# Kernel optimization log

Measured on AMD Instinct MI355X. Metric: run time of the kernel, lower is better.

The kernel has to match this reference:

```python
import jax, jax.numpy as jnp
import numpy as np

B, T, C, H = 65536, 100, 7, 2  # batch, timesteps, covariates, lstm hidden


def setup_inputs() -> dict:
    key = jax.random.key(0)
    ks = iter(jax.random.split(key, 32))
    def rn(shape, s=0.1):
        return jax.random.normal(next(ks), shape, dtype=jnp.float32) * s
    inp = {"x": jax.random.normal(next(ks), (B, T, C), dtype=jnp.float32)}
    for l, din in ((0, C), (1, 2 * H)):
        for suf in ("", "r"):
            inp[f"w_ih_l{l}{suf}"] = rn((4 * H, din))
            inp[f"w_hh_l{l}{suf}"] = rn((4 * H, H))
            inp[f"b_ih_l{l}{suf}"] = rn((4 * H,))
            inp[f"b_hh_l{l}{suf}"] = rn((4 * H,))
    inp["fc1_w"] = rn((64, 4 * T))
    inp["fc1_b"] = rn((64,))
    inp["fc2_w"] = rn((20, 64))
    inp["fc2_b"] = rn((20,))
    return inp


def _lstm_dir(xw, w_hh, b_hh, reverse):
    # xw: [T, B, 4H] precomputed input projection (x @ W_ih.T + b_ih)
    if reverse:
        xw = xw[::-1]
    h0 = jnp.zeros((xw.shape[1], H), xw.dtype)
    c0 = jnp.zeros((xw.shape[1], H), xw.dtype)

    def step(carry, gx):
        h, c = carry
        g = gx + h @ w_hh.T + b_hh            # [B, 4H]
        i, f, gg, o = jnp.split(g, 4, axis=-1)  # torch gate order i,f,g,o
        c = jax.nn.sigmoid(f) * c + jax.nn.sigmoid(i) * jnp.tanh(gg)
        h = jax.nn.sigmoid(o) * jnp.tanh(c)
        return (h, c), h

    _, hs = jax.lax.scan(step, (h0, c0), xw)
    if reverse:
        hs = hs[::-1]
    return hs  # [T, B, H]


def _bilstm_layer(x_tbf, w_ih_f, w_hh_f, b_ih_f, b_hh_f,
                  w_ih_b, w_hh_b, b_ih_b, b_hh_b):
    xw_f = jnp.einsum('tbc,gc->tbg', x_tbf, w_ih_f) + b_ih_f
    xw_b = jnp.einsum('tbc,gc->tbg', x_tbf, w_ih_b) + b_ih_b
    hf = _lstm_dir(xw_f, w_hh_f, b_hh_f, False)
    hb = _lstm_dir(xw_b, w_hh_b, b_hh_b, True)
    return jnp.concatenate([hf, hb], axis=-1)  # [T, B, 2H]


def reference(x,
              w_ih_l0, w_hh_l0, b_ih_l0, b_hh_l0,
              w_ih_l0r, w_hh_l0r, b_ih_l0r, b_hh_l0r,
              w_ih_l1, w_hh_l1, b_ih_l1, b_hh_l1,
              w_ih_l1r, w_hh_l1r, b_ih_l1r, b_hh_l1r,
              fc1_w, fc1_b, fc2_w, fc2_b):
    xt = jnp.transpose(x.reshape(-1, T, C), (1, 0, 2))  # [T, B, C] time-major
    h1 = _bilstm_layer(xt, w_ih_l0, w_hh_l0, b_ih_l0, b_hh_l0,
                       w_ih_l0r, w_hh_l0r, b_ih_l0r, b_hh_l0r)
    h2 = _bilstm_layer(h1, w_ih_l1, w_hh_l1, b_ih_l1, b_hh_l1,
                       w_ih_l1r, w_hh_l1r, b_ih_l1r, b_hh_l1r)
    out = jnp.transpose(h2, (1, 0, 2)).reshape(-1, 4 * T)  # flatten [B, 4T]
    out = jax.nn.relu(out)                  # relu BEFORE fc1, as in original
    out = jax.nn.relu(out @ fc1_w.T + fc1_b)
    return out @ fc2_w.T + fc2_b            # [B, 20]
```

## Files before the change

### kernel.cpp

```cpp
#include <hip/hip_runtime.h>

#define Bn 65536
#define Tn 100
#define Cn 7

typedef short short8 __attribute__((ext_vector_type(8)));
typedef float float4v __attribute__((ext_vector_type(4)));

__device__ __forceinline__ float fast_rcp(float x) { return __builtin_amdgcn_rcpf(x); }
__device__ __forceinline__ float sig_f(float x) { return fast_rcp(1.f + __expf(-x)); }
__device__ __forceinline__ float tanh_f(float x) { return 1.f - 2.f * fast_rcp(__expf(2.f * x) + 1.f); }
__device__ __forceinline__ unsigned bf16rne(float x) {
    unsigned u = __float_as_uint(x);
    return (u + 0x7fffu + ((u >> 16) & 1u)) >> 16;
}

typedef const __attribute__((address_space(1))) void* gp_t;
typedef __attribute__((address_space(3))) void* sp_t;
__device__ __forceinline__ void async_copy_dw(const float* g, float* l) {
    __builtin_amdgcn_global_load_lds((gp_t)g, (sp_t)l, 4, 0, 0);
}

__global__ void w2prep_kernel(const float* __restrict__ fc1_w, unsigned short* __restrict__ w2g) {
    int idx = blockIdx.x * 256 + threadIdx.x;
    int w = idx >> 13, d = (idx >> 12) & 1, n = (idx >> 6) & 63, kk = idx & 63;
    int tt = kk >> 1, i = kk & 1;
    int t = d ? (99 - 25 * w - tt) : (25 * w + tt);
    float v = (kk < 50) ? fc1_w[n * 400 + 4 * t + 2 * d + i] : 0.f;
    w2g[idx] = (unsigned short)bf16rne(v);
}

__global__ __launch_bounds__(256) void l0_kernel(
    const float* __restrict__ x,
    const float* __restrict__ wih_f, const float* __restrict__ whh_f,
    const float* __restrict__ bih_f, const float* __restrict__ bhh_f,
    const float* __restrict__ wih_r, const float* __restrict__ whh_r,
    const float* __restrict__ bih_r, const float* __restrict__ bhh_r,
    float2* __restrict__ h1f2)
{
    __shared__ float xs[2][2][4480];

    const int tid  = threadIdx.x;
    const int rev  = tid >> 7;
    const int s    = tid & 127;
    const int b    = blockIdx.x * 128 + s;
    const int w    = tid >> 6;
    const int lane = tid & 63;
    const int sdir = w >> 1;
    const int half = w & 1;

    const float* wih = rev ? wih_r : wih_f;
    const float* whh = rev ? whh_r : whh_f;
    const float* bih = rev ? bih_r : bih_f;
    const float* bhh = rev ? bhh_r : bhh_f;

    float wi[56], wh[16], bias[8];
#pragma unroll
    for (int k = 0; k < 56; ++k) wi[k] = wih[k];
#pragma unroll
    for (int k = 0; k < 16; ++k) wh[k] = whh[k];
#pragma unroll
    for (int k = 0; k < 8; ++k) bias[k] = bih[k] + bhh[k];

    const int e  = (lane >= 35) ? 1 : 0;
    const int r0 = lane - 35 * e;
    const int s0 = half * 64 + e;
    const float* xsamp = x + (size_t)(blockIdx.x * 128 + s0) * 700;

    auto stage = [&](int ch, int p) {
        const int off = sdir ? (665 - 35 * ch) : (35 * ch);
        const float* g = xsamp + off + r0;
        float* l = &xs[p][sdir][half * 2240 + lane];
        int r = r0;
#pragma unroll
        for (int i = 0; i < 35; ++i) {
            async_copy_dw(g, l);
            l += 64;
            const int c = (r >= 6) ? 1 : 0;
            g += c ? 1394 : 729;
            r += c ? -6 : 29;
        }
    };

    float h0 = 0.f, h1v = 0.f, c0 = 0.f, c1 = 0.f;

    stage(0, 0);
#pragma unroll 1
    for (int ch = 0; ch < 20; ++ch) {
        __builtin_amdgcn_s_waitcnt(0);
        __syncthreads();
        if (ch < 19) stage(ch + 1, (ch + 1) & 1);

        const int t0 = rev ? (95 - 5 * ch) : (5 * ch);
        const float* xbuf = &xs[ch & 1][rev][0];
#pragma unroll 1
        for (int tt = 0; tt < 5; ++tt) {
            const int rr = rev ? (4 - tt) : tt;
            const int t  = t0 + rr;
            const float* xrow = xbuf + s * 35 + rr * 7;

            float g[8];
#pragma unroll
            for (int k = 0; k < 8; ++k) g[k] = bias[k];
#pragma unroll
            for (int c = 0; c < 7; ++c) {
                const float xv = xrow[c];
#pragma unroll
                for (int k = 0; k < 8; ++k) g[k] = fmaf(wi[k * 7 + c], xv, g[k]);
            }
#pragma unroll
            for (int k = 0; k < 8; ++k)
                g[k] = fmaf(wh[k * 2], h0, fmaf(wh[k * 2 + 1], h1v, g[k]));

            const float i0 = sig_f(g[0]), i1 = sig_f(g[1]);
            const float f0 = sig_f(g[2]), f1 = sig_f(g[3]);
            const float q0 = tanh_f(g[4]), q1 = tanh_f(g[5]);
            const float o0 = sig_f(g[6]), o1 = sig_f(g[7]);
            c0 = fmaf(f0, c0, i0 * q0);
            c1 = fmaf(f1, c1, i1 * q1);
            h0  = o0 * tanh_f(c0);
            h1v = o1 * tanh_f(c1);

            h1f2[((size_t)t * 2 + rev) * Bn + b] = make_float2(h0, h1v);
        }
    }
}

__global__ __launch_bounds__(256) void l1fc_kernel(
    const float2* __restrict__ hin,
    const float* __restrict__ wih_f, const float* __restrict__ whh_f,
    const float* __restrict__ bih_f, const float* __restrict__ bhh_f,
    const float* __restrict__ wih_r, const float* __restrict__ whh_r,
    const float* __restrict__ bih_r, const float* __restrict__ bhh_r,
    const float4* __restrict__ w2g,
    const float* __restrict__ fc1_b,
    const float* __restrict__ fc2_w,
    const float* __restrict__ fc2_b,
    float* __restrict__ out)
{
    __shared__ unsigned a2[2 * 128 * 36];
    __shared__ unsigned w2[2 * 64 * 36];

    const int tid  = threadIdx.x;
    const int ww   = tid >> 6;
    const int lane = tid & 63;
    const int d    = ww >> 1;
    const int half = ww & 1;
    const int sm   = half * 64 + lane;
    const size_t b = (size_t)blockIdx.x * 128 + sm;

    const float* wih = d ? wih_r : wih_f;
    const float* whh = d ? whh_r : whh_f;
    const float* bih = d ? bih_r : bih_f;
    const float* bhh = d ? bhh_r : bhh_f;

    float wi[32], wh[16], bias[8];
#pragma unroll
    for (int k = 0; k < 32; ++k) wi[k] = wih[k];
#pragma unroll
    for (int k = 0; k < 16; ++k) wh[k] = whh[k];
#pragma unroll
    for (int k = 0; k < 8; ++k) bias[k] = bih[k] + bhh[k];

    float4v acc[2][4];
#pragma unroll
    for (int mt = 0; mt < 2; ++mt)
#pragma unroll
        for (int nt = 0; nt < 4; ++nt) acc[mt][nt] = (float4v){0.f, 0.f, 0.f, 0.f};

    for (int i2 = tid; i2 < 2 * 128 * 36; i2 += 256) a2[i2] = 0u;
    __syncthreads();

    auto tstep = [&](int st) { return d ? 99 - st : st; };
    auto hload = [&](int t, float2& uF, float2& uR) {
        uF = hin[((size_t)t * 2) * Bn + b];
        uR = hin[((size_t)t * 2 + 1) * Bn + b];
    };

    float2 aF, aR, p1F, p1R, p2F, p2R;
    hload(tstep(0), aF, aR);
    hload(tstep(1), p1F, p1R);
    hload(tstep(2), p2F, p2R);

    float h0 = 0.f, h1v = 0.f, c0 = 0.f, c1 = 0.f;
    const int cbase = tid * 4;

#pragma unroll 1
    for (int w = 0; w < 4; ++w) {
        float4 wl[4];
#pragma unroll
        for (int j = 0; j < 4; ++j) wl[j] = w2g[w * 1024 + cbase + j];

#pragma unroll 1
        for (int tt = 0; tt < 25; ++tt) {
            const int st = 25 * w + tt;
            const int sp = (st + 3 <= 99) ? st + 3 : 99;
            float2 nF, nR;
            hload(tstep(sp), nF, nR);

            float g[8];
#pragma unroll
            for (int k = 0; k < 8; ++k) {
                g[k] = bias[k];
                g[k] = fmaf(wi[k * 4 + 0], aF.x, g[k]);
                g[k] = fmaf(wi[k * 4 + 1], aF.y, g[k]);
                g[k] = fmaf(wi[k * 4 + 2], aR.x, g[k]);
                g[k] = fmaf(wi[k * 4 + 3], aR.y, g[k]);
                g[k] = fmaf(wh[k * 2], h0, fmaf(wh[k * 2 + 1], h1v, g[k]));
            }
            const float i0 = sig_f(g[0]), i1 = sig_f(g[1]);
            const float f0 = sig_f(g[2]), f1 = sig_f(g[3]);
            const float q0 = tanh_f(g[4]), q1 = tanh_f(g[5]);
            const float o0 = sig_f(g[6]), o1 = sig_f(g[7]);
            c0 = fmaf(f0, c0, i0 * q0);
            c1 = fmaf(f1, c1, i1 * q1);
            h0  = o0 * tanh_f(c0);
            h1v = o1 * tanh_f(c1);

            const unsigned vpk = bf16rne(fmaxf(h0, 0.f)) | (bf16rne(fmaxf(h1v, 0.f)) << 16);
            a2[d * 4608 + sm * 36 + tt] = vpk;

            aF = p1F; aR = p1R; p1F = p2F; p1R = p2R; p2F = nF; p2R = nR;
        }

#pragma unroll
        for (int j = 0; j < 4; ++j) {
            const int c = cbase + j;
            const int dst = (((c >> 9) << 6) + ((c >> 3) & 63)) * 36 + (c & 7) * 4;
            *(float4*)(&w2[dst]) = wl[j];
        }
        __syncthreads();

        {
            const int q = lane >> 4, l16 = lane & 15;
#pragma unroll
            for (int dd = 0; dd < 2; ++dd) {
#pragma unroll
                for (int kt = 0; kt < 2; ++kt) {
                    short8 av[2], bv[4];
#pragma unroll
                    for (int mt = 0; mt < 2; ++mt) {
                        const int srow = ww * 32 + mt * 16 + l16;
                        av[mt] = *(const short8*)&a2[dd * 4608 + srow * 36 + kt * 16 + q * 4];
                    }
#pragma unroll
                    for (int nt = 0; nt < 4; ++nt)
                        bv[nt] = *(const short8*)&w2[(dd * 64 + nt * 16 + l16) * 36 + kt * 16 + q * 4];
#pragma unroll
                    for (int mt = 0; mt < 2; ++mt)
#pragma unroll
                        for (int nt = 0; nt < 4; ++nt)
                            acc[mt][nt] = __builtin_amdgcn_mfma_f32_16x16x32_bf16(
                                av[mt], bv[nt], acc[mt][nt], 0, 0, 0);
                }
            }
        }
        __syncthreads();
    }

    {
        const int q = lane >> 4, l16 = lane & 15;
        float* eb = (float*)a2;
#pragma unroll
        for (int mt = 0; mt < 2; ++mt)
#pragma unroll
            for (int nt = 0; nt < 4; ++nt)
#pragma unroll
                for (int r = 0; r < 4; ++r) {
                    const int sl = ww * 32 + mt * 16 + q * 4 + r;
                    const int cl = nt * 16 + l16;
                    eb[sl * 65 + cl] = acc[mt][nt][r];
                }
    }
    __syncthreads();

    const float* eb = (const float*)a2;
    const int sm2 = tid & 127;
    const int og  = (tid >> 7) * 10;
    float z[64];
#pragma unroll
    for (int k = 0; k < 64; ++k) z[k] = fmaxf(eb[sm2 * 65 + k] + fc1_b[k], 0.f);
    float y[10];
#pragma unroll
    for (int o = 0; o < 10; ++o) {
        float r2 = fc2_b[og + o];
#pragma unroll
        for (int k = 0; k < 64; ++k) r2 = fmaf(fc2_w[(og + o) * 64 + k], z[k], r2);
        y[o] = r2;
    }
    __syncthreads();
    float* ebw = (float*)a2;
#pragma unroll
    for (int o = 0; o < 10; ++o) ebw[sm2 * 20 + og + o] = y[o];
    __syncthreads();
    for (int f = tid; f < 2560; f += 256)
        out[(size_t)blockIdx.x * 2560 + f] = ebw[f];
}

extern "C" void kernel_launch(void* const* d_in, const int* in_sizes, int n_in,
                              void* d_out, int out_size, void* d_ws, size_t ws_size,
                              hipStream_t stream) {
    const float* x = (const float*)d_in[0];
    const float* w_ih_l0  = (const float*)d_in[1];
    const float* w_hh_l0  = (const float*)d_in[2];
    const float* b_ih_l0  = (const float*)d_in[3];
    const float* b_hh_l0  = (const float*)d_in[4];
    const float* w_ih_l0r = (const float*)d_in[5];
    const float* w_hh_l0r = (const float*)d_in[6];
    const float* b_ih_l0r = (const float*)d_in[7];
    const float* b_hh_l0r = (const float*)d_in[8];
    const float* w_ih_l1  = (const float*)d_in[9];
    const float* w_hh_l1  = (const float*)d_in[10];
    const float* b_ih_l1  = (const float*)d_in[11];
    const float* b_hh_l1  = (const float*)d_in[12];
    const float* w_ih_l1r = (const float*)d_in[13];
    const float* w_hh_l1r = (const float*)d_in[14];
    const float* b_ih_l1r = (const float*)d_in[15];
    const float* b_hh_l1r = (const float*)d_in[16];
    const float* fc1_w = (const float*)d_in[17];
    const float* fc1_b = (const float*)d_in[18];
    const float* fc2_w = (const float*)d_in[19];
    const float* fc2_b = (const float*)d_in[20];

    float2* h1f2 = (float2*)d_ws;
    unsigned short* w2g = (unsigned short*)((char*)d_ws + (size_t)Tn * 4 * Bn * sizeof(float));

    w2prep_kernel<<<128, 256, 0, stream>>>(fc1_w, w2g);
    l0_kernel<<<512, 256, 0, stream>>>(x,
        w_ih_l0, w_hh_l0, b_ih_l0, b_hh_l0,
        w_ih_l0r, w_hh_l0r, b_ih_l0r, b_hh_l0r, h1f2);
    l1fc_kernel<<<512, 256, 0, stream>>>(h1f2,
        w_ih_l1, w_hh_l1, b_ih_l1, b_hh_l1,
        w_ih_l1r, w_hh_l1r, b_ih_l1r, b_hh_l1r,
        (const float4*)w2g, fc1_b, fc2_w, fc2_b, (float*)d_out);
}
```

Before: 468.7 us.

## Store layer-0 hidden states as bf16 and stage layer-1 inputs via async LDS copies

Layer-0 outputs are now packed as two bf16 values per 32-bit word, which halves the intermediate write and read traffic. Layer 1 now double-buffers its hidden-state and fc1-weight tiles in LDS using global_load_lds async copies, replacing the per-thread register prefetch of float2 values. The fc1 accumulation is reorganised into 10 windows of 10 timesteps, each using one K=32 MFMA per direction, which roughly doubles the zero-padded K work compared with the 4×25 split. The layer-0 waitcnt is relaxed so the next chunk's copy can overlap, and the extra bf16 rounding of layer-1 inputs adds some precision loss.

New measurement: 438.3 us. 1.07x faster.

```diff
diff --git a/kernel.cpp b/kernel.cpp
--- a/kernel.cpp
+++ b/kernel.cpp
@@ -14,19 +14,24 @@
     unsigned u = __float_as_uint(x);
     return (u + 0x7fffu + ((u >> 16) & 1u)) >> 16;
 }
+__device__ __forceinline__ float bf_lo(unsigned u) { return __uint_as_float(u << 16); }
+__device__ __forceinline__ float bf_hi(unsigned u) { return __uint_as_float(u & 0xffff0000u); }
 
 typedef const __attribute__((address_space(1))) void* gp_t;
 typedef __attribute__((address_space(3))) void* sp_t;
-__device__ __forceinline__ void async_copy_dw(const float* g, float* l) {
+__device__ __forceinline__ void async_copy_dw(const void* g, void* l) {
     __builtin_amdgcn_global_load_lds((gp_t)g, (sp_t)l, 4, 0, 0);
 }
 
 __global__ void w2prep_kernel(const float* __restrict__ fc1_w, unsigned short* __restrict__ w2g) {
     int idx = blockIdx.x * 256 + threadIdx.x;
-    int w = idx >> 13, d = (idx >> 12) & 1, n = (idx >> 6) & 63, kk = idx & 63;
+    int w  = idx >> 12;
+    int d  = (idx >> 11) & 1;
+    int n  = (idx >> 5) & 63;
+    int kk = idx & 31;
     int tt = kk >> 1, i = kk & 1;
-    int t = d ? (99 - 25 * w - tt) : (25 * w + tt);
-    float v = (kk < 50) ? fc1_w[n * 400 + 4 * t + 2 * d + i] : 0.f;
+    int t  = d ? (99 - 10 * w - tt) : (10 * w + tt);
+    float v = (kk < 20) ? fc1_w[n * 400 + 4 * t + 2 * d + i] : 0.f;
     w2g[idx] = (unsigned short)bf16rne(v);
 }
 
@@ -36,7 +41,7 @@
     const float* __restrict__ bih_f, const float* __restrict__ bhh_f,
     const float* __restrict__ wih_r, const float* __restrict__ whh_r,
     const float* __restrict__ bih_r, const float* __restrict__ bhh_r,
-    float2* __restrict__ h1f2)
+    unsigned* __restrict__ h1u)
 {
     __shared__ float xs[2][2][4480];
 
@@ -87,9 +92,11 @@
     stage(0, 0);
 #pragma unroll 1
     for (int ch = 0; ch < 20; ++ch) {
-        __builtin_amdgcn_s_waitcnt(0);
+        if (ch == 0) __builtin_amdgcn_s_waitcnt(0x0F70);
+        else         __builtin_amdgcn_s_waitcnt(0x0F75);
         __syncthreads();
         if (ch < 19) stage(ch + 1, (ch + 1) & 1);
+        __builtin_amdgcn_sched_barrier(0);
 
         const int t0 = rev ? (95 - 5 * ch) : (5 * ch);
         const float* xbuf = &xs[ch & 1][rev][0];
@@ -121,25 +128,27 @@
             h0  = o0 * tanh_f(c0);
             h1v = o1 * tanh_f(c1);
 
-            h1f2[((size_t)t * 2 + rev) * Bn + b] = make_float2(h0, h1v);
+            h1u[((size_t)t * 2 + rev) * Bn + b] = bf16rne(h0) | (bf16rne(h1v) << 16);
         }
     }
 }
 
 __global__ __launch_bounds__(256) void l1fc_kernel(
-    const float2* __restrict__ hin,
+    const unsigned* __restrict__ hin,
     const float* __restrict__ wih_f, const float* __restrict__ whh_f,
     const float* __restrict__ bih_f, const float* __restrict__ bhh_f,
     const float* __restrict__ wih_r, const float* __restrict__ whh_r,
     const float* __restrict__ bih_r, const float* __restrict__ bhh_r,
-    const float4* __restrict__ w2g,
+    const unsigned* __restrict__ w2g,
     const float* __restrict__ fc1_b,
     const float* __restrict__ fc2_w,
     const float* __restrict__ fc2_b,
     float* __restrict__ out)
 {
-    __shared__ unsigned a2[2 * 128 * 36];
-    __shared__ unsigned w2[2 * 64 * 36];
+    __shared__ unsigned smem[19456];
+    unsigned* a2  = smem;
+    unsigned* w2b = smem + 5120;
+    unsigned* hst = smem + 9216;
 
     const int tid  = threadIdx.x;
     const int ww   = tid >> 6;
@@ -147,7 +156,7 @@
     const int d    = ww >> 1;
     const int half = ww & 1;
     const int sm   = half * 64 + lane;
-    const size_t b = (size_t)blockIdx.x * 128 + sm;
+    const int b0   = blockIdx.x * 128;
 
     const float* wih = d ? wih_r : wih_f;
     const float* whh = d ? whh_r : whh_f;
@@ -168,44 +177,58 @@
 #pragma unroll
         for (int nt = 0; nt < 4; ++nt) acc[mt][nt] = (float4v){0.f, 0.f, 0.f, 0.f};
 
-    for (int i2 = tid; i2 < 2 * 128 * 36; i2 += 256) a2[i2] = 0u;
-    __syncthreads();
-
-    auto tstep = [&](int st) { return d ? 99 - st : st; };
-    auto hload = [&](int t, float2& uF, float2& uR) {
-        uF = hin[((size_t)t * 2) * Bn + b];
-        uR = hin[((size_t)t * 2 + 1) * Bn + b];
+    for (int i = tid; i < 5120; i += 256) a2[i] = 0u;
+
+    auto stage_h = [&](int w, int pb) {
+        unsigned* dst = hst + pb * 5120;
+        const int Rb = tid >> 7;
+        const int s  = tid & 127;
+#pragma unroll
+        for (int i = 0; i < 20; ++i) {
+            const int R  = Rb + 2 * i;
+            const int dd = (R >= 20) ? 1 : 0;
+            const int r2 = R - 20 * dd;
+            const int p  = (r2 >= 10) ? 1 : 0;
+            const int j  = r2 - 10 * p;
+            const int t  = dd ? (99 - (10 * w + j)) : (10 * w + j);
+            async_copy_dw(hin + ((size_t)t * 2 + p) * Bn + b0 + s, dst + R * 128 + s);
+        }
     };
-
-    float2 aF, aR, p1F, p1R, p2F, p2R;
-    hload(tstep(0), aF, aR);
-    hload(tstep(1), p1F, p1R);
-    hload(tstep(2), p2F, p2R);
+    auto stage_w = [&](int w, int pb) {
+        const unsigned* src = w2g + w * 2048;
+        unsigned* dst = w2b + pb * 2048;
+#pragma unroll
+        for (int i = 0; i < 8; ++i)
+            async_copy_dw(src + i * 256 + tid, dst + i * 256 + tid);
+    };
+
+    stage_h(0, 0); stage_w(0, 0);
 
     float h0 = 0.f, h1v = 0.f, c0 = 0.f, c1 = 0.f;
-    const int cbase = tid * 4;
+    const int q = lane >> 4, l16 = lane & 15;
 
 #pragma unroll 1
-    for (int w = 0; w < 4; ++w) {
-        float4 wl[4];
-#pragma unroll
-        for (int j = 0; j < 4; ++j) wl[j] = w2g[w * 1024 + cbase + j];
-
+    for (int w = 0; w < 10; ++w) {
+        __builtin_amdgcn_s_waitcnt(0x0F70);
+        __syncthreads();
+        if (w < 9) { stage_h(w + 1, (w + 1) & 1); stage_w(w + 1, (w + 1) & 1); }
+
+        const unsigned* hb = hst + (w & 1) * 5120 + d * 2560;
 #pragma unroll 1
-        for (int tt = 0; tt < 25; ++tt) {
-            const int st = 25 * w + tt;
-            const int sp = (st + 3 <= 99) ? st + 3 : 99;
-            float2 nF, nR;
-            hload(tstep(sp), nF, nR);
+        for (int j = 0; j < 10; ++j) {
+            const unsigned uF = hb[j * 128 + sm];
+            const unsigned uR = hb[1280 + j * 128 + sm];
+            const float aF0 = bf_lo(uF), aF1 = bf_hi(uF);
+            const float aR0 = bf_lo(uR), aR1 = bf_hi(uR);
 
             float g[8];
 #pragma unroll
             for (int k = 0; k < 8; ++k) {
                 g[k] = bias[k];
-                g[k] = fmaf(wi[k * 4 + 0], aF.x, g[k]);
-                g[k] = fmaf(wi[k * 4 + 1], aF.y, g[k]);
-                g[k] = fmaf(wi[k * 4 + 2], aR.x, g[k]);
-                g[k] = fmaf(wi[k * 4 + 3], aR.y, g[k]);
+                g[k] = fmaf(wi[k * 4 + 0], aF0, g[k]);
+                g[k] = fmaf(wi[k * 4 + 1], aF1, g[k]);
+                g[k] = fmaf(wi[k * 4 + 2], aR0, g[k]);
+                g[k] = fmaf(wi[k * 4 + 3], aR1, g[k]);
                 g[k] = fmaf(wh[k * 2], h0, fmaf(wh[k * 2 + 1], h1v, g[k]));
             }
             const float i0 = sig_f(g[0]), i1 = sig_f(g[1]);
@@ -217,50 +240,34 @@
             h0  = o0 * tanh_f(c0);
             h1v = o1 * tanh_f(c1);
 
-            const unsigned vpk = bf16rne(fmaxf(h0, 0.f)) | (bf16rne(fmaxf(h1v, 0.f)) << 16);
-            a2[d * 4608 + sm * 36 + tt] = vpk;
-
-            aF = p1F; aR = p1R; p1F = p2F; p1R = p2R; p2F = nF; p2R = nR;
-        }
-
-#pragma unroll
-        for (int j = 0; j < 4; ++j) {
-            const int c = cbase + j;
-            const int dst = (((c >> 9) << 6) + ((c >> 3) & 63)) * 36 + (c & 7) * 4;
-            *(float4*)(&w2[dst]) = wl[j];
+            a2[d * 2560 + sm * 20 + j] = bf16rne(fmaxf(h0, 0.f)) | (bf16rne(fmaxf(h1v, 0.f)) << 16);
         }
         __syncthreads();
 
         {
-            const int q = lane >> 4, l16 = lane & 15;
+            const unsigned* wb = w2b + (w & 1) * 2048;
 #pragma unroll
             for (int dd = 0; dd < 2; ++dd) {
-#pragma unroll
-                for (int kt = 0; kt < 2; ++kt) {
-                    short8 av[2], bv[4];
-#pragma unroll
-                    for (int mt = 0; mt < 2; ++mt) {
-                        const int srow = ww * 32 + mt * 16 + l16;
-                        av[mt] = *(const short8*)&a2[dd * 4608 + srow * 36 + kt * 16 + q * 4];
-                    }
+                short8 av[2], bv[4];
+#pragma unroll
+                for (int mt = 0; mt < 2; ++mt)
+                    av[mt] = *(const short8*)&a2[dd * 2560 + (ww * 32 + mt * 16 + l16) * 20 + q * 4];
+#pragma unroll
+                for (int nt = 0; nt < 4; ++nt)
+                    bv[nt] = *(const short8*)&wb[dd * 1024 + (nt * 16 + l16) * 16 + q * 4];
+#pragma unroll
+                for (int mt = 0; mt < 2; ++mt)
 #pragma unroll
                     for (int nt = 0; nt < 4; ++nt)
-                        bv[nt] = *(const short8*)&w2[(dd * 64 + nt * 16 + l16) * 36 + kt * 16 + q * 4];
-#pragma unroll
-                    for (int mt = 0; mt < 2; ++mt)
-#pragma unroll
-                        for (int nt = 0; nt < 4; ++nt)
-                            acc[mt][nt] = __builtin_amdgcn_mfma_f32_16x16x32_bf16(
-                                av[mt], bv[nt], acc[mt][nt], 0, 0, 0);
-                }
+                        acc[mt][nt] = __builtin_amdgcn_mfma_f32_16x16x32_bf16(
+                            av[mt], bv[nt], acc[mt][nt], 0, 0, 0);
             }
         }
-        __syncthreads();
     }
+    __syncthreads();
 
     {
-        const int q = lane >> 4, l16 = lane & 15;
-        float* eb = (float*)a2;
+        float* eb = (float*)smem;
 #pragma unroll
         for (int mt = 0; mt < 2; ++mt)
 #pragma unroll
@@ -274,7 +281,7 @@
     }
     __syncthreads();
 
-    const float* eb = (const float*)a2;
+    const float* eb = (const float*)smem;
     const int sm2 = tid & 127;
     const int og  = (tid >> 7) * 10;
     float z[64];
@@ -289,7 +296,7 @@
         y[o] = r2;
     }
     __syncthreads();
-    float* ebw = (float*)a2;
+    float* ebw = (float*)smem;
 #pragma unroll
     for (int o = 0; o < 10; ++o) ebw[sm2 * 20 + og + o] = y[o];
     __syncthreads();
@@ -322,15 +329,15 @@
     const float* fc2_w = (const float*)d_in[19];
     const float* fc2_b = (const float*)d_in[20];
 
-    float2* h1f2 = (float2*)d_ws;
-    unsigned short* w2g = (unsigned short*)((char*)d_ws + (size_t)Tn * 4 * Bn * sizeof(float));
-
-    w2prep_kernel<<<128, 256, 0, stream>>>(fc1_w, w2g);
+    unsigned* h1u = (unsigned*)d_ws;
+    unsigned short* w2g = (unsigned short*)((char*)d_ws + (size_t)Tn * 2 * Bn * 4);
+
+    w2prep_kernel<<<160, 256, 0, stream>>>(fc1_w, w2g);
     l0_kernel<<<512, 256, 0, stream>>>(x,
         w_ih_l0, w_hh_l0, b_ih_l0, b_hh_l0,
-        w_ih_l0r, w_hh_l0r, b_ih_l0r, b_hh_l0r, h1f2);
-    l1fc_kernel<<<512, 256, 0, stream>>>(h1f2,
+        w_ih_l0r, w_hh_l0r, b_ih_l0r, b_hh_l0r, h1u);
+    l1fc_kernel<<<512, 256, 0, stream>>>(h1u,
         w_ih_l1, w_hh_l1, b_ih_l1, b_hh_l1,
         w_ih_l1r, w_hh_l1r, b_ih_l1r, b_hh_l1r,
-        (const float4*)w2g, fc1_b, fc2_w, fc2_b, (float*)d_out);
-}
+        (const unsigned*)w2g, fc1_b, fc2_w, fc2_b, (float*)d_out);
+}
```
